# Performance work log

Measured on AMD Instinct MI355X. Metric: run time of the kernel, lower is better.

## Reference

```python
import jax, jax.numpy as jnp
import numpy as np

HEADS = 8
HIDDEN = 1536
HEAD_DIM = HIDDEN // HEADS
SCALE = HEAD_DIM ** -0.5


def setup_inputs() -> dict:
    key = jax.random.key(0)
    ks = jax.random.split(key, 10)
    B, S_IMG, S_TXT = 32, 1024, 77
    w = 0.02
    return {
        "img": jax.random.normal(ks[0], (B, S_IMG, HIDDEN), dtype=jnp.float32),
        "text": jax.random.normal(ks[1], (B, S_TXT, HIDDEN), dtype=jnp.float32),
        "Wq": jax.random.normal(ks[2], (HIDDEN, HIDDEN), dtype=jnp.float32) * w,
        "bq": jnp.zeros((HIDDEN,), dtype=jnp.float32),
        "Wk": jax.random.normal(ks[3], (HIDDEN, HIDDEN), dtype=jnp.float32) * w,
        "bk": jnp.zeros((HIDDEN,), dtype=jnp.float32),
        "Wv": jax.random.normal(ks[4], (HIDDEN, HIDDEN), dtype=jnp.float32) * w,
        "bv": jnp.zeros((HIDDEN,), dtype=jnp.float32),
        "Wo": jax.random.normal(ks[5], (HIDDEN, HIDDEN), dtype=jnp.float32) * w,
        "bo": jnp.zeros((HIDDEN,), dtype=jnp.float32),
    }


def reference(img, text, Wq, bq, Wk, bk, Wv, bv, Wo, bo):
    B, Sq, D = img.shape
    Sk = text.shape[1]
    # QKV projections (nn.Linear: y = x @ W.T + b)
    q = img @ Wq.T + bq    # [B, Sq, D]
    k = text @ Wk.T + bk   # [B, Sk, D]
    v = text @ Wv.T + bv
    # detach trick: position 0 of k/v has gradient stopped; forward value unchanged
    k0 = jax.lax.stop_gradient(k[:, :1, :])
    k = jnp.concatenate([k0, k[:, 1:, :]], axis=1)
    v0 = jax.lax.stop_gradient(v[:, :1, :])
    v = jnp.concatenate([v0, v[:, 1:, :]], axis=1)
    # split heads
    q = q.reshape(B, Sq, HEADS, HEAD_DIM)
    k = k.reshape(B, Sk, HEADS, HEAD_DIM)
    v = v.reshape(B, Sk, HEADS, HEAD_DIM)
    # attention scores and probs (mask is None in this module)
    scores = jnp.einsum("bqhd,bkhd->bhqk", q, k) * SCALE  # [B, H, Sq, Sk]
    probs = jax.nn.softmax(scores, axis=-1)
    out = jnp.einsum("bhqk,bkhd->bqhd", probs, v).reshape(B, Sq, D)
    return out @ Wo.T + bo
```

## Files before the change

kernel.cpp:

```cpp
#include <hip/hip_runtime.h>
#include <hip/hip_bf16.h>


typedef unsigned short u16;
typedef _Float16 f16x8 __attribute__((ext_vector_type(8)));
typedef __attribute__((ext_vector_type(8))) short s16x8;
typedef __attribute__((ext_vector_type(4))) float f32x4;
typedef __attribute__((ext_vector_type(4))) short s16x4;

#define MFMAH(a, b, c) __builtin_amdgcn_mfma_f32_16x16x32_f16(a, b, c, 0, 0, 0)

__device__ __forceinline__ u16 f2h(float x) {
    _Float16 h = (_Float16)x;
    return __builtin_bit_cast(u16, h);
}

__device__ __forceinline__ void gload16(const u16* g, const u16* l) {
    __builtin_amdgcn_global_load_lds(
        (const __attribute__((address_space(1))) unsigned int*)g,
        (__attribute__((address_space(3))) unsigned int*)l, 16, 0, 0);
}

__device__ __forceinline__ unsigned ldsa(const u16* p) {
    return (unsigned)(size_t)(const __attribute__((address_space(3))) u16*)p;
}

__device__ __forceinline__ f16x8 dsr128(unsigned byte_addr) {
    f16x8 d;
    asm volatile("ds_read_b128 %0, %1" : "=v"(d) : "v"(byte_addr));
    return d;
}

__device__ __forceinline__ int rh(int r) { return (r >> 1) & 3; }

__global__ void conv_h(const float* __restrict__ x, u16* __restrict__ h, int n8) {
    const int i = blockIdx.x * 256 + threadIdx.x;
    if (i >= n8) return;
    const f32x4 a = ((const f32x4*)x)[2 * i];
    const f32x4 b = ((const f32x4*)x)[2 * i + 1];
    u16 o[8];
#pragma unroll
    for (int j = 0; j < 4; ++j) { o[j] = f2h(a[j]); o[4 + j] = f2h(b[j]); }
    *(s16x8*)&h[(size_t)i << 3] = *(s16x8*)o;
}

struct Conv5Args {
    const float* x[5];
    u16* h[5];
    int n8[5];
};

__global__ void conv_h5(Conv5Args A) {
    const int z = blockIdx.y;
    const int i = blockIdx.x * 256 + threadIdx.x;
    if (i >= A.n8[z]) return;
    const float* x = A.x[z];
    const f32x4 a = ((const f32x4*)x)[2 * i];
    const f32x4 b = ((const f32x4*)x)[2 * i + 1];
    u16 o[8];
#pragma unroll
    for (int j = 0; j < 4; ++j) { o[j] = f2h(a[j]); o[4 + j] = f2h(b[j]); }
    *(s16x8*)&A.h[z][(size_t)i << 3] = *(s16x8*)o;
}

template <int OUTF32>
__global__ __launch_bounds__(512, 2) void gemm_h_nt(
    const u16* __restrict__ A,
    const u16* __restrict__ B0, const float* __restrict__ bias0, void* __restrict__ C0,
    const u16* __restrict__ B1, const float* __restrict__ bias1, void* __restrict__ C1,
    int M, int N, int K, int nby) {
    __shared__ u16 lds[65536];

    const u16* B = B0; const float* bias = bias0; void* Cout = C0;
    if (blockIdx.z) { B = B1; bias = bias1; Cout = C1; }

    const int nwg = gridDim.x;
    const int q8 = nwg >> 3, r8 = nwg & 7;
    const int xcd = blockIdx.x & 7, loc = blockIdx.x >> 3;
    const int wgid = (xcd < r8 ? xcd * (q8 + 1) : r8 * (q8 + 1) + (xcd - r8) * q8) + loc;
    const int bx = wgid / nby, by = wgid - bx * nby;
    const int row0 = bx * 256, col0 = by * 256;

    const int t = threadIdx.x, lane = t & 63, w = t >> 6;
    const int wr = w >> 2, wc = w & 3;
    const int l15 = lane & 15, lhi = lane >> 4;

    const u16* gpA[2]; const u16* gpB[2];
    int lofA[2], lofB[2];
#pragma unroll
    for (int it = 0; it < 2; ++it) {
        const int ci = it * 512 + t;
        const int row = ci >> 2, slot = ci & 3;
        const int gs = slot ^ rh(row);
        int ar = row0 + row; if (ar > M - 1) ar = M - 1;
        gpA[it] = A + (size_t)ar * K + (gs << 3);
        gpB[it] = B + (size_t)(col0 + row) * K + (gs << 3);
        lofA[it] = ci * 8;
        lofB[it] = 8192 + ci * 8;
    }

    const int ss = rh(l15);
    const unsigned lb0 = ldsa(lds);
    unsigned aof[8], bof[4];
#pragma unroll
    for (int i = 0; i < 8; ++i) {
        const int ar = wr * 128 + i * 16 + l15;
        aof[i] = (unsigned)((ar * 32 + ((lhi ^ ss) << 3)) * 2);
    }
#pragma unroll
    for (int n = 0; n < 4; ++n) {
        const int br = wc * 64 + n * 16 + l15;
        bof[n] = (unsigned)((8192 + br * 32 + ((lhi ^ ss) << 3)) * 2);
    }

    f32x4 acc[8][4] = {};
    const int NT = K >> 5;

#define SBAR0() __builtin_amdgcn_sched_barrier(0)
#define BARX()  do { SBAR0(); __builtin_amdgcn_s_barrier(); SBAR0(); } while (0)

#pragma unroll
    for (int p = 0; p < 3; ++p) {
        const size_t kp = (size_t)p << 5;
        u16* lb = lds + (p << 14);
        gload16(gpA[0] + kp, lb + lofA[0]); gload16(gpA[1] + kp, lb + lofA[1]);
        gload16(gpB[0] + kp, lb + lofB[0]); gload16(gpB[1] + kp, lb + lofB[1]);
    }
    asm volatile("s_waitcnt vmcnt(4)" ::: "memory");
    BARX();

    f16x8 al[4], ah[4], bb[4];
#pragma unroll
    for (int nf = 0; nf < 4; ++nf) bb[nf] = dsr128(lb0 + bof[nf]);
#pragma unroll
    for (int mf = 0; mf < 4; ++mf) al[mf] = dsr128(lb0 + aof[mf]);
    SBAR0();

    for (int tt = 0; tt < NT; ++tt) {
        const unsigned cb = lb0 + ((unsigned)(tt & 3) << 15);
        const unsigned nb = lb0 + ((unsigned)((tt + 1) & 3) << 15);
        u16* lsb = lds + (((tt + 3) & 3) << 14);
        const int tx = (tt + 3 < NT) ? tt + 3 : tt + 3 - NT;
        const size_t kn = (size_t)tx << 5;

        gload16(gpA[0] + kn, lsb + lofA[0]);
        gload16(gpA[1] + kn, lsb + lofA[1]);
#pragma unroll
        for (int mf = 0; mf < 4; ++mf) ah[mf] = dsr128(cb + aof[4 + mf]);
        SBAR0();
        asm volatile("s_waitcnt lgkmcnt(4)" ::: "memory");
        SBAR0();
        __builtin_amdgcn_s_setprio(1);
#pragma unroll
        for (int nf = 0; nf < 4; ++nf)
#pragma unroll
            for (int mf = 0; mf < 4; ++mf)
                acc[mf][nf] = MFMAH(al[mf], bb[nf], acc[mf][nf]);
        __builtin_amdgcn_s_setprio(0);
#pragma unroll
        for (int mf = 0; mf < 4; ++mf) al[mf] = dsr128(nb + aof[mf]);
        SBAR0();
        gload16(gpB[0] + kn, lsb + lofB[0]);
        gload16(gpB[1] + kn, lsb + lofB[1]);
        asm volatile("s_waitcnt lgkmcnt(4)" ::: "memory");
        SBAR0();
        __builtin_amdgcn_s_setprio(1);
#pragma unroll
        for (int nf = 0; nf < 4; ++nf)
#pragma unroll
            for (int mf = 0; mf < 4; ++mf)
                acc[4 + mf][nf] = MFMAH(ah[mf], bb[nf], acc[4 + mf][nf]);
        __builtin_amdgcn_s_setprio(0);
#pragma unroll
        for (int nf = 0; nf < 4; ++nf) bb[nf] = dsr128(nb + bof[nf]);
        SBAR0();
        asm volatile("s_waitcnt vmcnt(4)" ::: "memory");
        BARX();
    }
    asm volatile("s_waitcnt vmcnt(0) lgkmcnt(0)" ::: "memory");

#pragma unroll
    for (int nf = 0; nf < 4; ++nf) {
        const int col = col0 + wc * 64 + nf * 16 + l15;
        const float bs = bias[col];
#pragma unroll
        for (int mf = 0; mf < 8; ++mf) {
            const int row = row0 + wr * 128 + mf * 16 + (lhi << 2);
#pragma unroll
            for (int r = 0; r < 4; ++r) {
                if (row + r < M) {
                    const float v = acc[mf][nf][r] + bs;
                    if (OUTF32) ((float*)Cout)[(size_t)(row + r) * N + col] = v;
                    else        ((u16*)Cout)[(size_t)(row + r) * N + col] = f2h(v);
                }
            }
        }
    }
#undef SBAR0
#undef BARX
}

#define ALDK 200
#define ALDP 104

__global__ void attn_fused(const u16* __restrict__ qbuf, const u16* __restrict__ kbuf,
                           const u16* __restrict__ vbuf, u16* __restrict__ obuf) {
    __shared__ u16 Ks[80 * ALDK];
    __shared__ u16 Pls[64 * ALDP];
    __shared__ u16 Vt[96 * ALDP];

    const int t = threadIdx.x, lane = t & 63, w = t >> 6;
    const int qt = blockIdx.x, h = blockIdx.y, b = blockIdx.z;
    const int l15 = lane & 15, lhi = lane >> 4;

    f16x8 qf[6];
    {
        const size_t qrow = (size_t)(b * 1024 + qt * 64 + w * 16 + l15);
        const u16* qp = qbuf + qrow * 1536 + h * 192 + (lhi << 3);
#pragma unroll
        for (int kt = 0; kt < 6; ++kt) qf[kt] = *(const f16x8*)(qp + kt * 32);
    }

    for (int c = t; c < 80 * 24; c += 256) {
        const int s = c / 24, d8 = (c - s * 24) << 3;
        s16x8 val = {};
        if (s < 77) val = *(const s16x8*)&kbuf[(size_t)(b * 77 + s) * 1536 + h * 192 + d8];
        *(s16x8*)&Ks[s * ALDK + d8] = val;
    }
    for (int c = t; c < 96 * 12; c += 256) {
        const int s = c % 96, d8 = (c / 96) << 3;
        s16x8 val = {};
        if (s < 77) val = *(const s16x8*)&vbuf[(size_t)(b * 77 + s) * 1536 + h * 192 + d8];
#pragma unroll
        for (int j = 0; j < 8; ++j) Vt[(d8 + j) * ALDP + s] = (u16)val[j];
    }
    {
        const int row = w * 16 + l15;
        s16x4 z = {0, 0, 0, 0};
        *(s16x4*)&Pls[row * ALDP + 80 + (lhi << 2)] = z;
    }
    __syncthreads();

    f32x4 sacc[5] = {};
#pragma unroll
    for (int kt = 0; kt < 6; ++kt) {
#pragma unroll
        for (int nf = 0; nf < 5; ++nf) {
            f16x8 kf = *(const f16x8*)&Ks[(nf * 16 + l15) * ALDK + kt * 32 + (lhi << 3)];
            sacc[nf] = MFMAH(qf[kt], kf, sacc[nf]);
        }
    }

    float rps[4];
    const float scale = 0.07216878364870323f;
#pragma unroll
    for (int r = 0; r < 4; ++r) {
        float m = -1e30f;
#pragma unroll
        for (int nf = 0; nf < 5; ++nf) {
            const int c = nf * 16 + l15;
            const float sv = sacc[nf][r] * scale;
            if (c < 77) m = fmaxf(m, sv);
        }
#pragma unroll
        for (int off = 1; off < 16; off <<= 1) m = fmaxf(m, __shfl_xor(m, off));
        float sum = 0.f;
#pragma unroll
        for (int nf = 0; nf < 5; ++nf) {
            const int c = nf * 16 + l15;
            const float p = (c < 77) ? __expf(sacc[nf][r] * scale - m) : 0.f;
            sacc[nf][r] = p;
            sum += p;
        }
#pragma unroll
        for (int off = 1; off < 16; off <<= 1) sum += __shfl_xor(sum, off);
        rps[r] = 1.0f / sum;
    }

#pragma unroll
    for (int r = 0; r < 4; ++r)
#pragma unroll
        for (int nf = 0; nf < 5; ++nf)
            Pls[(w * 16 + (lhi << 2) + r) * ALDP + nf * 16 + l15] = f2h(sacc[nf][r]);
    __syncthreads();

    f16x8 pa[3];
#pragma unroll
    for (int kt = 0; kt < 3; ++kt)
        pa[kt] = *(const f16x8*)&Pls[(w * 16 + l15) * ALDP + kt * 32 + (lhi << 3)];

    const size_t orow = (size_t)(b * 1024 + qt * 64 + w * 16 + (lhi << 2));

    {
        f32x4 oacc[6] = {};
#pragma unroll
        for (int kt = 0; kt < 3; ++kt)
#pragma unroll
            for (int nf = 0; nf < 6; ++nf) {
                f16x8 vf = *(const f16x8*)&Vt[(nf * 16 + l15) * ALDP + kt * 32 + (lhi << 3)];
                oacc[nf] = MFMAH(pa[kt], vf, oacc[nf]);
            }
#pragma unroll
        for (int nf = 0; nf < 6; ++nf) {
            const int col = h * 192 + nf * 16 + l15;
#pragma unroll
            for (int r = 0; r < 4; ++r)
                obuf[(orow + r) * 1536 + col] = f2h(oacc[nf][r] * rps[r]);
        }
    }
    __syncthreads();
    for (int c = t; c < 96 * 12; c += 256) {
        const int s = c % 96, d8 = (c / 96) << 3;
        s16x8 val = {};
        if (s < 77) val = *(const s16x8*)&vbuf[(size_t)(b * 77 + s) * 1536 + h * 192 + 96 + d8];
#pragma unroll
        for (int j = 0; j < 8; ++j) Vt[(d8 + j) * ALDP + s] = (u16)val[j];
    }
    __syncthreads();
    {
        f32x4 oacc[6] = {};
#pragma unroll
        for (int kt = 0; kt < 3; ++kt)
#pragma unroll
            for (int nf = 0; nf < 6; ++nf) {
                f16x8 vf = *(const f16x8*)&Vt[(nf * 16 + l15) * ALDP + kt * 32 + (lhi << 3)];
                oacc[nf] = MFMAH(pa[kt], vf, oacc[nf]);
            }
#pragma unroll
        for (int nf = 0; nf < 6; ++nf) {
            const int col = h * 192 + 96 + nf * 16 + l15;
#pragma unroll
            for (int r = 0; r < 4; ++r)
                obuf[(orow + r) * 1536 + col] = f2h(oacc[nf][r] * rps[r]);
        }
    }
}

extern "C" void kernel_launch(void* const* d_in, const int* in_sizes, int n_in,
                              void* d_out, int out_size, void* d_ws, size_t ws_size,
                              hipStream_t stream) {
    const float* img  = (const float*)d_in[0];
    const float* text = (const float*)d_in[1];
    const float* Wq   = (const float*)d_in[2];
    const float* bq   = (const float*)d_in[3];
    const float* Wk   = (const float*)d_in[4];
    const float* bk   = (const float*)d_in[5];
    const float* Wv   = (const float*)d_in[6];
    const float* bv   = (const float*)d_in[7];
    const float* Wo   = (const float*)d_in[8];
    const float* bo   = (const float*)d_in[9];

    const size_t imgN = (size_t)32768 * 1536;
    const size_t txtN = (size_t)2464 * 1536;
    const size_t wN   = (size_t)1536 * 1536;

    u16* img_h = (u16*)d_ws;
    u16* qb    = img_h + imgN;
    u16* txt_h = qb + imgN;
    u16* Wq_h  = txt_h + txtN;
    u16* Wk_h  = Wq_h + wN;
    u16* Wv_h  = Wk_h + wN;
    u16* Wo_h  = Wv_h + wN;
    u16* kb    = Wo_h + wN;
    u16* vb    = kb + txtN;

    hipLaunchKernelGGL(conv_h, dim3((unsigned)(imgN / 8 / 256)), dim3(256),
                       0, stream, img, img_h, (int)(imgN / 8));
    Conv5Args ca;
    ca.x[0] = text; ca.h[0] = txt_h; ca.n8[0] = (int)(txtN / 8);
    ca.x[1] = Wq;   ca.h[1] = Wq_h;  ca.n8[1] = (int)(wN / 8);
    ca.x[2] = Wk;   ca.h[2] = Wk_h;  ca.n8[2] = (int)(wN / 8);
    ca.x[3] = Wv;   ca.h[3] = Wv_h;  ca.n8[3] = (int)(wN / 8);
    ca.x[4] = Wo;   ca.h[4] = Wo_h;  ca.n8[4] = (int)(wN / 8);
    hipLaunchKernelGGL(conv_h5, dim3((unsigned)((txtN / 8 + 255) / 256), 5),
                       dim3(256), 0, stream, ca);

    hipLaunchKernelGGL((gemm_h_nt<0>), dim3(768), dim3(512), 0, stream,
                       img_h, Wq_h, bq, (void*)qb, Wq_h, bq, (void*)qb,
                       32768, 1536, 1536, 6);
    hipLaunchKernelGGL((gemm_h_nt<0>), dim3(60, 1, 2), dim3(512), 0, stream,
                       txt_h, Wk_h, bk, (void*)kb, Wv_h, bv, (void*)vb,
                       2464, 1536, 1536, 6);
    hipLaunchKernelGGL(attn_fused, dim3(16, 8, 32), dim3(256), 0, stream,
                       qb, kb, vb, qb);
    hipLaunchKernelGGL((gemm_h_nt<1>), dim3(768), dim3(512), 0, stream,
                       qb, Wo_h, bo, d_out, Wo_h, bo, d_out,
                       32768, 1536, 1536, 6);
}
```

Measured before the change: 606.4 us.

## Fuse img fp32-to-fp16 conversion into QKV GEMM and merge Q/K/V launches

```diff
diff --git a/kernel.cpp b/kernel.cpp
--- a/kernel.cpp
+++ b/kernel.cpp
@@ -32,17 +32,6 @@
 }
 
 __device__ __forceinline__ int rh(int r) { return (r >> 1) & 3; }
-
-__global__ void conv_h(const float* __restrict__ x, u16* __restrict__ h, int n8) {
-    const int i = blockIdx.x * 256 + threadIdx.x;
-    if (i >= n8) return;
-    const f32x4 a = ((const f32x4*)x)[2 * i];
-    const f32x4 b = ((const f32x4*)x)[2 * i + 1];
-    u16 o[8];
-#pragma unroll
-    for (int j = 0; j < 4; ++j) { o[j] = f2h(a[j]); o[4 + j] = f2h(b[j]); }
-    *(s16x8*)&h[(size_t)i << 3] = *(s16x8*)o;
-}
 
 struct Conv5Args {
     const float* x[5];
@@ -61,6 +50,138 @@
 #pragma unroll
     for (int j = 0; j < 4; ++j) { o[j] = f2h(a[j]); o[4 + j] = f2h(b[j]); }
     *(s16x8*)&A.h[z][(size_t)i << 3] = *(s16x8*)o;
+}
+
+__global__ __launch_bounds__(512, 2) void qkv_gemm(
+    const float* __restrict__ imgF, const u16* __restrict__ txtH,
+    const u16* __restrict__ Wq, const u16* __restrict__ Wk, const u16* __restrict__ Wv,
+    const float* __restrict__ bq, const float* __restrict__ bk, const float* __restrict__ bv,
+    u16* __restrict__ qb, u16* __restrict__ kb, u16* __restrict__ vb) {
+    constexpr int K = 1536;
+    const int z = blockIdx.z;
+    const int nwg = z ? 60 : 768;
+    if ((int)blockIdx.x >= nwg) return;
+    const int M = z ? 2464 : 32768;
+    const u16* B = (z == 0) ? Wq : (z == 1 ? Wk : Wv);
+    const float* bias = (z == 0) ? bq : (z == 1 ? bk : bv);
+    u16* Cout = (z == 0) ? qb : (z == 1 ? kb : vb);
+
+    __shared__ u16 lds[32768];
+
+    const int q8 = nwg >> 3, r8 = nwg & 7;
+    const int xcd = blockIdx.x & 7, loc = blockIdx.x >> 3;
+    const int wgid = (xcd < r8 ? xcd * (q8 + 1) : r8 * (q8 + 1) + (xcd - r8) * q8) + loc;
+    const int bx = wgid / 6, by = wgid - bx * 6;
+    const int row0 = bx * 256, col0 = by * 256;
+
+    const int t = threadIdx.x, lane = t & 63, w = t >> 6;
+    const int wr = w >> 2, wc = w & 3;
+    const int l15 = lane & 15, lhi = lane >> 4;
+
+    const float* gfA[2];
+    const u16* gpA[2];
+    const u16* gpB[2];
+    int lofA[2], lofB[2];
+#pragma unroll
+    for (int it = 0; it < 2; ++it) {
+        const int ci = it * 512 + t;
+        const int row = ci >> 2, slot = ci & 3;
+        const int gs = slot ^ rh(row);
+        int ar = row0 + row; if (ar > M - 1) ar = M - 1;
+        gfA[it] = imgF + (size_t)ar * K + (gs << 3);
+        gpA[it] = txtH + (size_t)ar * K + (gs << 3);
+        gpB[it] = B + (size_t)(col0 + row) * K + (gs << 3);
+        lofA[it] = ci * 8;
+        lofB[it] = 8192 + ci * 8;
+    }
+
+    const int ss = rh(l15);
+    int aof[8], bof[4];
+#pragma unroll
+    for (int i = 0; i < 8; ++i) {
+        const int ar = wr * 128 + i * 16 + l15;
+        aof[i] = ar * 32 + ((lhi ^ ss) << 3);
+    }
+#pragma unroll
+    for (int n = 0; n < 4; ++n) {
+        const int br = wc * 64 + n * 16 + l15;
+        bof[n] = 8192 + br * 32 + ((lhi ^ ss) << 3);
+    }
+
+    f32x4 acc[8][4] = {};
+    const int NT = K >> 5;
+
+    f32x4 af[2][2];
+#define LOADAF(kk) do { \
+        af[0][0] = *(const f32x4*)(gfA[0] + (kk)); \
+        af[0][1] = *(const f32x4*)(gfA[0] + (kk) + 4); \
+        af[1][0] = *(const f32x4*)(gfA[1] + (kk)); \
+        af[1][1] = *(const f32x4*)(gfA[1] + (kk) + 4); } while (0)
+#define WRITEA(bufo) do { \
+        _Pragma("unroll") for (int it = 0; it < 2; ++it) { \
+            u16 hh[8]; \
+            _Pragma("unroll") for (int j = 0; j < 4; ++j) { \
+                hh[j] = f2h(af[it][0][j]); hh[4 + j] = f2h(af[it][1][j]); } \
+            *(s16x8*)&lds[(bufo) + lofA[it]] = *(s16x8*)hh; } } while (0)
+
+    if (z == 0) {
+        LOADAF(0);
+        WRITEA(0);
+        LOADAF(32);
+    } else {
+        gload16(gpA[0], lds + lofA[0]);
+        gload16(gpA[1], lds + lofA[1]);
+    }
+    gload16(gpB[0], lds + lofB[0]);
+    gload16(gpB[1], lds + lofB[1]);
+
+    for (int tt = 0; tt < NT; ++tt) {
+        const int cb = (tt & 1) << 14;
+        const int nb = ((tt & 1) ^ 1) << 14;
+        __syncthreads();
+
+        if (tt + 1 < NT) {
+            const size_t kn = (size_t)(tt + 1) << 5;
+            if (z == 0) {
+                WRITEA(nb);
+                const size_t kn2 = (tt + 2 < NT) ? ((size_t)(tt + 2) << 5) : 0;
+                LOADAF(kn2);
+            } else {
+                gload16(gpA[0] + kn, lds + nb + lofA[0]);
+                gload16(gpA[1] + kn, lds + nb + lofA[1]);
+            }
+            gload16(gpB[0] + kn, lds + nb + lofB[0]);
+            gload16(gpB[1] + kn, lds + nb + lofB[1]);
+        }
+
+        f16x8 a[8];
+#pragma unroll
+        for (int mf = 0; mf < 8; ++mf) a[mf] = *(const f16x8*)&lds[cb + aof[mf]];
+#pragma unroll
+        for (int nf = 0; nf < 4; ++nf) {
+            const f16x8 bfr = *(const f16x8*)&lds[cb + bof[nf]];
+#pragma unroll
+            for (int mf = 0; mf < 8; ++mf)
+                acc[mf][nf] = MFMAH(a[mf], bfr, acc[mf][nf]);
+        }
+    }
+#undef LOADAF
+#undef WRITEA
+
+#pragma unroll
+    for (int nf = 0; nf < 4; ++nf) {
+        const int col = col0 + wc * 64 + nf * 16 + l15;
+        const float bs = bias[col];
+#pragma unroll
+        for (int mf = 0; mf < 8; ++mf) {
+            const int row = row0 + wr * 128 + mf * 16 + (lhi << 2);
+#pragma unroll
+            for (int r = 0; r < 4; ++r) {
+                if (row + r < M)
+                    Cout[(size_t)(row + r) * 1536 + col] = f2h(acc[mf][nf][r] + bs);
+            }
+        }
+    }
 }
 
 template <int OUTF32>
@@ -236,8 +357,8 @@
     }
     {
         const int row = w * 16 + l15;
-        s16x4 z = {0, 0, 0, 0};
-        *(s16x4*)&Pls[row * ALDP + 80 + (lhi << 2)] = z;
+        s16x4 zz = {0, 0, 0, 0};
+        *(s16x4*)&Pls[row * ALDP + 80 + (lhi << 2)] = zz;
     }
     __syncthreads();
 
@@ -354,8 +475,7 @@
     const size_t txtN = (size_t)2464 * 1536;
     const size_t wN   = (size_t)1536 * 1536;
 
-    u16* img_h = (u16*)d_ws;
-    u16* qb    = img_h + imgN;
+    u16* qb    = (u16*)d_ws;
     u16* txt_h = qb + imgN;
     u16* Wq_h  = txt_h + txtN;
     u16* Wk_h  = Wq_h + wN;
@@ -364,8 +484,6 @@
     u16* kb    = Wo_h + wN;
     u16* vb    = kb + txtN;
 
-    hipLaunchKernelGGL(conv_h, dim3((unsigned)(imgN / 8 / 256)), dim3(256),
-                       0, stream, img, img_h, (int)(imgN / 8));
     Conv5Args ca;
     ca.x[0] = text; ca.h[0] = txt_h; ca.n8[0] = (int)(txtN / 8);
     ca.x[1] = Wq;   ca.h[1] = Wq_h;  ca.n8[1] = (int)(wN / 8);
@@ -375,14 +493,12 @@
     hipLaunchKernelGGL(conv_h5, dim3((unsigned)((txtN / 8 + 255) / 256), 5),
                        dim3(256), 0, stream, ca);
 
-    hipLaunchKernelGGL((gemm_h_nt<0>), dim3(768), dim3(512), 0, stream,
-                       img_h, Wq_h, bq, (void*)qb, Wq_h, bq, (void*)qb,
-                       32768, 1536, 1536, 6);
-    hipLaunchKernelGGL((gemm_h_nt<0>), dim3(60, 1, 2), dim3(512), 0, stream,
-                       txt_h, Wk_h, bk, (void*)kb, Wv_h, bv, (void*)vb,
-                       2464, 1536, 1536, 6);
+    hipLaunchKernelGGL(qkv_gemm, dim3(768, 1, 3), dim3(512), 0, stream,
+                       img, txt_h, Wq_h, Wk_h, Wv_h, bq, bk, bv, qb, kb, vb);
+
     hipLaunchKernelGGL(attn_fused, dim3(16, 8, 32), dim3(256), 0, stream,
                        qb, kb, vb, qb);
+
     hipLaunchKernelGGL((gemm_h_nt<1>), dim3(768), dim3(512), 0, stream,
                        qb, Wo_h, bo, d_out, Wo_h, bo, d_out,
                        32768, 1536, 1536, 6);
```

Result: faster. 592.3 us (-2.3%).
